# Kernel optimization log

Measured on AMD Instinct MI355X. Metric: run time of the kernel, lower is better.

The kernel has to match this reference:

```python
import jax, jax.numpy as jnp
import numpy as np

D_MODEL = 2048
N_HEADS = 32
N_KV_HEADS = 8
D_K = D_MODEL // N_HEADS          # 64
N_REP = N_HEADS // N_KV_HEADS     # 4
KV_DIM = N_KV_HEADS * D_K         # 512
B, T = 4, 2048


def setup_inputs() -> dict:
    key = jax.random.key(0)
    ks = jax.random.split(key, 9)
    s_in = 1.0 / np.sqrt(D_MODEL)
    x = jax.random.normal(ks[0], (B, T, D_MODEL), dtype=jnp.float32)
    Wq = jax.random.uniform(ks[1], (D_MODEL, D_MODEL), jnp.float32, -s_in, s_in)
    bq = jax.random.uniform(ks[2], (D_MODEL,), jnp.float32, -s_in, s_in)
    Wk = jax.random.uniform(ks[3], (D_MODEL, KV_DIM), jnp.float32, -s_in, s_in)
    bk = jax.random.uniform(ks[4], (KV_DIM,), jnp.float32, -s_in, s_in)
    Wv = jax.random.uniform(ks[5], (D_MODEL, KV_DIM), jnp.float32, -s_in, s_in)
    bv = jax.random.uniform(ks[6], (KV_DIM,), jnp.float32, -s_in, s_in)
    Wo = jax.random.uniform(ks[7], (D_MODEL, D_MODEL), jnp.float32, -s_in, s_in)
    bo = jax.random.uniform(ks[8], (D_MODEL,), jnp.float32, -s_in, s_in)
    return {"x": x, "Wq": Wq, "bq": bq, "Wk": Wk, "bk": bk,
            "Wv": Wv, "bv": bv, "Wo": Wo, "bo": bo}


def reference(x, Wq, bq, Wk, bk, Wv, bv, Wo, bo):
    Bsz, S, _ = x.shape
    # projections
    q = x @ Wq + bq                                   # (B, T, d_model)
    k = x @ Wk + bk                                   # (B, T, kv_dim)
    v = x @ Wv + bv
    # (B, n_kv, n_rep, T, d_k) for q; (B, n_kv, T, d_k) for k, v.
    # Grouping q by kv head avoids materializing repeated K/V.
    q = q.reshape(Bsz, S, N_KV_HEADS, N_REP, D_K).transpose(0, 2, 3, 1, 4)
    k = k.reshape(Bsz, S, N_KV_HEADS, D_K).transpose(0, 2, 1, 3)
    v = v.reshape(Bsz, S, N_KV_HEADS, D_K).transpose(0, 2, 1, 3)
    scale = 1.0 / np.sqrt(D_K).astype(np.float32)
    scores = jnp.einsum('bgrtd,bgsd->bgrts', q, k) * scale  # (B, n_kv, n_rep, T, T)
    causal = jnp.tril(jnp.ones((S, S), dtype=bool))
    scores = jnp.where(causal, scores, jnp.finfo(scores.dtype).min)
    p = jax.nn.softmax(scores, axis=-1)
    o = jnp.einsum('bgrts,bgsd->bgrtd', p, v)               # (B, n_kv, n_rep, T, d_k)
    o = o.transpose(0, 3, 1, 2, 4).reshape(Bsz, S, D_MODEL)
    return o @ Wo + bo
```

## Files before the change

### kernel.cpp

```cpp
#include <hip/hip_runtime.h>
#include <cstdint>
#include <cstddef>

typedef __attribute__((ext_vector_type(8))) short short8;
typedef __attribute__((ext_vector_type(4))) float f32x4;

#define D_MODEL 2048
#define KV_DIM  512
#define N_HEADS 32
#define N_KV    8
#define D_K     64
#define B_SZ    4
#define T_SEQ   2048
#define M_TOT   (B_SZ * T_SEQ)
#define N1      (D_MODEL + 2 * KV_DIM)
#define NEG_BIG (-1e30f)
#define Q_PRESCALE 0.18033688011112042f

__device__ __forceinline__ unsigned short f2bf(float f) {
    union { float f; unsigned int i; } c; c.f = f;
    unsigned int u = c.i;
    u += 0x7FFFu + ((u >> 16) & 1u);
    return (unsigned short)(u >> 16);
}

__device__ __forceinline__ unsigned int cvtpk_bf16(float lo, float hi) {
    unsigned int r;
    asm("v_cvt_pk_bf16_f32 %0, %1, %2" : "=v"(r) : "v"(lo), "v"(hi));
    return r;
}

__device__ __forceinline__ float e2(float x) {
    float r;
    asm("v_exp_f32 %0, %1" : "=v"(r) : "v"(x));
    return r;
}

__device__ __forceinline__ void async16(unsigned short* lds, const unsigned short* g) {
    __builtin_amdgcn_global_load_lds(
        (const __attribute__((address_space(1))) unsigned int*)g,
        (__attribute__((address_space(3))) unsigned int*)lds, 16, 0, 0);
}

__global__ __launch_bounds__(256)
void stage_x(const float* __restrict__ x, unsigned short* __restrict__ xb, int n) {
    for (int i = blockIdx.x * blockDim.x + threadIdx.x; i * 4 < n;
         i += gridDim.x * blockDim.x) {
        const f32x4 v = *(const f32x4*)&x[i * 4];
        unsigned short o[4];
#pragma unroll
        for (int k = 0; k < 4; k++) o[k] = f2bf(v[k]);
        *(uint64_t*)&xb[i * 4] = *(const uint64_t*)o;
    }
}

__global__ __launch_bounds__(256)
void transpose_f32_bf16(const float* __restrict__ src,
                        unsigned short* __restrict__ dst, int R, int C) {
    __shared__ unsigned short tile[32][34];
    int bx = blockIdx.x * 32;
    int by = blockIdx.y * 32;
    int tx = threadIdx.x;
    int ty = threadIdx.y;
#pragma unroll
    for (int i = 0; i < 32; i += 8)
        tile[ty + i][tx] = f2bf(src[(size_t)(by + ty + i) * C + bx + tx]);
    __syncthreads();
#pragma unroll
    for (int i = 0; i < 32; i += 8)
        dst[(size_t)(bx + ty + i) * R + by + tx] = tile[tx][ty + i];
}

template <int MODE>
__global__ __launch_bounds__(256)
void gemm_bt(const unsigned short* __restrict__ A,
             const unsigned short* __restrict__ Bt,
             const float* __restrict__ b0,
             const float* __restrict__ b1,
             const float* __restrict__ b2,
             unsigned short* __restrict__ out0,
             unsigned short* __restrict__ out1,
             unsigned short* __restrict__ out2,
             float* __restrict__ outF,
             int K) {
    __shared__ __align__(16) unsigned short As[128 * 32];
    __shared__ __align__(16) unsigned short Bs[128 * 32];

    const int t    = threadIdx.x;
    const int wave = t >> 6;
    const int lane = t & 63;
    const int quad = lane >> 4;
    const int l16  = lane & 15;
    const int wm   = (wave >> 1) * 64;
    const int wn   = (wave & 1) * 64;
    const int rowBase = blockIdx.y * 128;
    const int colBase = blockIdx.x * 128;

    f32x4 acc[4][4];
#pragma unroll
    for (int i = 0; i < 4; i++)
#pragma unroll
        for (int j = 0; j < 4; j++)
            acc[i][j] = (f32x4){0.f, 0.f, 0.f, 0.f};

    const int r0  = t >> 2;
    const int off = (t & 3) * 8;
    const unsigned short* Ap = A  + (size_t)(rowBase + r0) * K + off;
    const unsigned short* Bp = Bt + (size_t)(colBase + r0) * K + off;
    const size_t rowStep = (size_t)64 * K;

    for (int k0 = 0; k0 < K; k0 += 32) {
        *(short8*)&As[t * 8]         = *(const short8*)(Ap + k0);
        *(short8*)&As[(t + 256) * 8] = *(const short8*)(Ap + rowStep + k0);
        *(short8*)&Bs[t * 8]         = *(const short8*)(Bp + k0);
        *(short8*)&Bs[(t + 256) * 8] = *(const short8*)(Bp + rowStep + k0);
        __syncthreads();

        short8 af[4], bfr[4];
#pragma unroll
        for (int i = 0; i < 4; i++)
            af[i] = *(const short8*)&As[(wm + i * 16 + l16) * 32 + quad * 8];
#pragma unroll
        for (int i = 0; i < 4; i++)
            bfr[i] = *(const short8*)&Bs[(wn + i * 16 + l16) * 32 + quad * 8];

#pragma unroll
        for (int mi = 0; mi < 4; mi++)
#pragma unroll
            for (int ni = 0; ni < 4; ni++)
                acc[mi][ni] = __builtin_amdgcn_mfma_f32_16x16x32_bf16(
                    af[mi], bfr[ni], acc[mi][ni], 0, 0, 0);
        __syncthreads();
    }

#pragma unroll
    for (int mi = 0; mi < 4; mi++) {
        const int rowT = rowBase + wm + mi * 16 + quad * 4;
#pragma unroll
        for (int ni = 0; ni < 4; ni++) {
            const int col = colBase + wn + ni * 16 + l16;
#pragma unroll
            for (int r = 0; r < 4; r++) {
                float v = acc[mi][ni][r];
                const int rr = rowT + r;
                if (MODE == 0) {
                    if (col < D_MODEL) {
                        v = (v + b0[col]) * Q_PRESCALE;
                        out0[(size_t)rr * D_MODEL + col] = f2bf(v);
                    } else if (col < D_MODEL + KV_DIM) {
                        const int c = col - D_MODEL;
                        v += b1[c];
                        out1[(size_t)rr * KV_DIM + c] = f2bf(v);
                    } else {
                        const int c = col - (D_MODEL + KV_DIM);
                        v += b2[c];
                        const int b   = rr >> 11;
                        const int tt  = rr & 2047;
                        const int kvh = c >> 6;
                        const int d   = c & 63;
                        out2[((size_t)((b * N_KV + kvh) * D_K + d)) * T_SEQ + tt] = f2bf(v);
                    }
                } else {
                    v += b0[col];
                    outF[(size_t)rr * D_MODEL + col] = v;
                }
            }
        }
    }
}

__global__ __launch_bounds__(512)
void attn_fwd(const unsigned short* __restrict__ qb,
              const unsigned short* __restrict__ kb,
              const unsigned short* __restrict__ vt,
              unsigned short* __restrict__ ob) {
    __shared__ __align__(16) unsigned short Ks[4][64 * 64];
    __shared__ __align__(16) unsigned short Vs[4][64 * 64];

    const int t    = threadIdx.x;
    const int wave = t >> 6;
    const int lane = t & 63;
    const int quad = lane >> 4;
    const int l16  = lane & 15;
    const int qt   = (int)gridDim.x - 1 - (int)blockIdx.x;
    const int h    = blockIdx.y;
    const int b    = blockIdx.z;
    const int kvh  = h >> 2;
    const int qBase = qt * 256;
    const int rowG  = b * T_SEQ;
    const size_t vtBase = (size_t)(b * N_KV + kvh) * D_K * T_SEQ;

    short8 qf[2][2];
#pragma unroll
    for (int mi = 0; mi < 2; mi++) {
        const int row = rowG + qBase + wave * 32 + mi * 16 + l16;
#pragma unroll
        for (int kk = 0; kk < 2; kk++)
            qf[mi][kk] = *(const short8*)&qb[(size_t)row * D_MODEL + h * D_K + kk * 32 + quad * 8];
    }

    f32x4 oacc[2][4];
#pragma unroll
    for (int i = 0; i < 2; i++)
#pragma unroll
        for (int j = 0; j < 4; j++)
            oacc[i][j] = (f32x4){0.f, 0.f, 0.f, 0.f};
    float m_run[2], l_run[2];
#pragma unroll
    for (int i = 0; i < 2; i++) { m_run[i] = NEG_BIG; l_run[i] = 0.f; }

    const int rr  = t >> 3;
    const int sc8 = ((t & 7) ^ (rr & 7)) << 3;

    auto stage = [&](int bi, int sB) {
        async16(&Ks[bi][wave * 8 * 64],
                kb + (size_t)(rowG + sB + rr) * KV_DIM + kvh * D_K + sc8);
        async16(&Vs[bi][wave * 8 * 64],
                vt + vtBase + (size_t)rr * T_SEQ + sB + sc8);
    };

    const int jMax = 4 * qt + 3;

    stage(0, 0);
    stage(1, 64);
    stage(2, 128);

    for (int j = 0; j <= jMax; ++j) {
        const int rem = jMax - j;
        if (rem >= 2)      asm volatile("s_waitcnt vmcnt(4)" ::: "memory");
        else if (rem == 1) asm volatile("s_waitcnt vmcnt(2)" ::: "memory");
        else               asm volatile("s_waitcnt vmcnt(0)" ::: "memory");
        __builtin_amdgcn_s_barrier();
        __builtin_amdgcn_sched_barrier(0);

        if (rem >= 3) stage((j + 3) & 3, (j + 3) * 64);

        const int sRel = j * 64 - qBase;
        const bool skip   = sRel > wave * 32 + 31;
        const bool doMask = sRel + 63 > wave * 32;

        if (!skip) {
            const int bi = j & 3;
            const char* KsB = (const char*)&Ks[bi][0];
            const char* VsB = (const char*)&Vs[bi][0];
            const int swz   = (l16 & 7) << 4;

            f32x4 sacc[4][2];
            __builtin_amdgcn_s_setprio(1);
#pragma unroll
            for (int ni = 0; ni < 4; ni++) {
                const int rowB = (ni * 16 + l16) * 128;
                const short8 kf0 = *(const short8*)(KsB + rowB + ((quad * 16) ^ swz));
                const short8 kf1 = *(const short8*)(KsB + rowB + ((64 + quad * 16) ^ swz));
#pragma unroll
                for (int mi = 0; mi < 2; mi++) {
                    f32x4 s = (f32x4){0.f, 0.f, 0.f, 0.f};
                    s = __builtin_amdgcn_mfma_f32_16x16x32_bf16(kf0, qf[mi][0], s, 0, 0, 0);
                    s = __builtin_amdgcn_mfma_f32_16x16x32_bf16(kf1, qf[mi][1], s, 0, 0, 0);
                    sacc[ni][mi] = s;
                }
            }
            __builtin_amdgcn_s_setprio(0);

            uint2 packed[4][2];
#pragma unroll
            for (int mi = 0; mi < 2; mi++) {
                float tm = NEG_BIG;
#pragma unroll
                for (int ni = 0; ni < 4; ni++)
#pragma unroll
                    for (int r = 0; r < 4; r++) {
                        float v = sacc[ni][mi][r];
                        if (doMask) {
                            const int kc = sRel + ni * 16 + quad * 4 + r;
                            const int qr = wave * 32 + mi * 16 + l16;
                            if (kc > qr) v = NEG_BIG;
                        }
                        sacc[ni][mi][r] = v;
                        tm = fmaxf(tm, v);
                    }
                tm = fmaxf(tm, __shfl_xor(tm, 16));
                tm = fmaxf(tm, __shfl_xor(tm, 32));

                float mref = m_run[mi];
                float mnew, alpha;
                if (__all(tm <= mref + 11.0f)) {
                    mnew = mref; alpha = 1.f;
                } else {
                    mnew  = fmaxf(mref, tm);
                    alpha = e2(mref - mnew);
                    m_run[mi] = mnew;
#pragma unroll
                    for (int r2 = 0; r2 < 4; r2++) {
                        const float aR = __shfl(alpha, (lane & 48) + quad * 4 + r2);
#pragma unroll
                        for (int di = 0; di < 4; di++) oacc[mi][di][r2] *= aR;
                    }
                }
                float rs = 0.f;
#pragma unroll
                for (int ni = 0; ni < 4; ni++) {
#pragma unroll
                    for (int r = 0; r < 4; r++) {
                        const float p = e2(sacc[ni][mi][r] - mnew);
                        sacc[ni][mi][r] = p;
                        rs += p;
                    }
                    packed[ni][mi].x = cvtpk_bf16(sacc[ni][mi][0], sacc[ni][mi][1]);
                    packed[ni][mi].y = cvtpk_bf16(sacc[ni][mi][2], sacc[ni][mi][3]);
                }
                rs += __shfl_xor(rs, 16);
                rs += __shfl_xor(rs, 32);
                l_run[mi] = l_run[mi] * alpha + rs;
            }

#pragma unroll
            for (int ks = 0; ks < 2; ks++) {
                short8 pa[2];
#pragma unroll
                for (int mi = 0; mi < 2; mi++) {
                    const int srcA = ((quad & 1) << 5) + l16;
                    const uint2 pL = packed[2 * ks][mi];
                    const uint2 pH = packed[2 * ks + 1][mi];
                    const unsigned a0x = __shfl((int)pL.x, srcA);
                    const unsigned a0y = __shfl((int)pL.y, srcA);
                    const unsigned b0x = __shfl((int)pL.x, srcA + 16);
                    const unsigned b0y = __shfl((int)pL.y, srcA + 16);
                    const unsigned a1x = __shfl((int)pH.x, srcA);
                    const unsigned a1y = __shfl((int)pH.y, srcA);
                    const unsigned b1x = __shfl((int)pH.x, srcA + 16);
                    const unsigned b1y = __shfl((int)pH.y, srcA + 16);
                    const int hi = quad >> 1;
                    union { unsigned u[4]; short8 s; } pw;
                    pw.u[0] = hi ? a1x : a0x;
                    pw.u[1] = hi ? a1y : a0y;
                    pw.u[2] = hi ? b1x : b0x;
                    pw.u[3] = hi ? b1y : b0y;
                    pa[mi] = pw.s;
                }
                __builtin_amdgcn_s_setprio(1);
#pragma unroll
                for (int di = 0; di < 4; di++) {
                    const short8 vb = *(const short8*)(VsB + (di * 16 + l16) * 128 +
                                                      ((ks * 64 + quad * 16) ^ swz));
#pragma unroll
                    for (int mi = 0; mi < 2; mi++)
                        oacc[mi][di] = __builtin_amdgcn_mfma_f32_16x16x32_bf16(
                            pa[mi], vb, oacc[mi][di], 0, 0, 0);
                }
                __builtin_amdgcn_s_setprio(0);
            }
        }
    }

#pragma unroll
    for (int mi = 0; mi < 2; mi++) {
#pragma unroll
        for (int r = 0; r < 4; r++) {
            const float lr  = __shfl(l_run[mi], (lane & 48) + quad * 4 + r);
            const float inv = 1.f / lr;
            const int row = rowG + qBase + wave * 32 + mi * 16 + quad * 4 + r;
#pragma unroll
            for (int di = 0; di < 4; di++)
                ob[(size_t)row * D_MODEL + h * D_K + di * 16 + l16] =
                    f2bf(oacc[mi][di][r] * inv);
        }
    }
}

extern "C" void kernel_launch(void* const* d_in, const int* in_sizes, int n_in,
                              void* d_out, int out_size, void* d_ws, size_t ws_size,
                              hipStream_t stream) {
    const float* x  = (const float*)d_in[0];
    const float* Wq = (const float*)d_in[1];
    const float* bq = (const float*)d_in[2];
    const float* Wk = (const float*)d_in[3];
    const float* bk = (const float*)d_in[4];
    const float* Wv = (const float*)d_in[5];
    const float* bv = (const float*)d_in[6];
    const float* Wo = (const float*)d_in[7];
    const float* bo = (const float*)d_in[8];
    float* out = (float*)d_out;

    char* ws = (char*)d_ws;
    unsigned short* qb   = (unsigned short*)(ws);
    unsigned short* Wbuf = (unsigned short*)(ws + 33554432);
    unsigned short* xb   = (unsigned short*)(ws + 46137344);
    unsigned short* kb   = (unsigned short*)d_out;
    unsigned short* vt   = (unsigned short*)d_out + 4194304;

    stage_x<<<4096, 256, 0, stream>>>(x, xb, 16777216);

    dim3 tb(32, 8);
    transpose_f32_bf16<<<dim3(64, 64), tb, 0, stream>>>(Wq, Wbuf, 2048, 2048);
    transpose_f32_bf16<<<dim3(16, 64), tb, 0, stream>>>(Wk, Wbuf + 2048 * 2048, 2048, 512);
    transpose_f32_bf16<<<dim3(16, 64), tb, 0, stream>>>(Wv, Wbuf + 2560 * 2048, 2048, 512);

    gemm_bt<0><<<dim3(N1 / 128, M_TOT / 128), 256, 0, stream>>>(
        xb, Wbuf, bq, bk, bv, qb, kb, vt, nullptr, D_MODEL);

    transpose_f32_bf16<<<dim3(64, 64), tb, 0, stream>>>(Wo, Wbuf, 2048, 2048);

    attn_fwd<<<dim3(T_SEQ / 256, N_HEADS, B_SZ), 512, 0, stream>>>(qb, kb, vt, qb);

    gemm_bt<1><<<dim3(D_MODEL / 128, M_TOT / 128), 256, 0, stream>>>(
        qb, Wbuf, bo, nullptr, nullptr, nullptr, nullptr, nullptr, out, D_MODEL);
}
```

Before: 755.1 us.

## Remove P-operand shuffles by permuting V k-index layout, tree-reduce softmax max/sum

The probability tile was being redistributed across lanes with eight __shfl calls per MFMA operand so it matched the PV MFMA A-layout. Now each lane's own packed P values are used directly as the A operand, and the V B-operand is gathered as two 8-byte LDS reads so its k index lines up with that permuted P layout. Row max and row sum are also computed as balanced trees instead of serial chains to shorten dependency latency. This removes cross-lane permute traffic in exchange for twice as many, narrower LDS reads for V, which may raise LDS bank pressure given the swizzle.

```diff
diff --git a/kernel.cpp b/kernel.cpp
--- a/kernel.cpp
+++ b/kernel.cpp
@@ -265,20 +265,26 @@
             uint2 packed[4][2];
 #pragma unroll
             for (int mi = 0; mi < 2; mi++) {
-                float tm = NEG_BIG;
+                float v[16];
 #pragma unroll
                 for (int ni = 0; ni < 4; ni++)
 #pragma unroll
                     for (int r = 0; r < 4; r++) {
-                        float v = sacc[ni][mi][r];
+                        float x = sacc[ni][mi][r];
                         if (doMask) {
                             const int kc = sRel + ni * 16 + quad * 4 + r;
                             const int qr = wave * 32 + mi * 16 + l16;
-                            if (kc > qr) v = NEG_BIG;
+                            if (kc > qr) x = NEG_BIG;
                         }
-                        sacc[ni][mi][r] = v;
-                        tm = fmaxf(tm, v);
+                        v[ni * 4 + r] = x;
                     }
+                float m8[8];
+#pragma unroll
+                for (int i = 0; i < 8; i++) m8[i] = fmaxf(v[i], v[i + 8]);
+                float m4[4];
+#pragma unroll
+                for (int i = 0; i < 4; i++) m4[i] = fmaxf(m8[i], m8[i + 4]);
+                float tm = fmaxf(fmaxf(m4[0], m4[1]), fmaxf(m4[2], m4[3]));
                 tm = fmaxf(tm, __shfl_xor(tm, 16));
                 tm = fmaxf(tm, __shfl_xor(tm, 32));
 
@@ -297,21 +303,24 @@
                         for (int di = 0; di < 4; di++) oacc[mi][di][r2] *= aR;
                     }
                 }
-                float rs = 0.f;
-#pragma unroll
-                for (int ni = 0; ni < 4; ni++) {
-#pragma unroll
-                    for (int r = 0; r < 4; r++) {
-                        const float p = e2(sacc[ni][mi][r] - mnew);
-                        sacc[ni][mi][r] = p;
-                        rs += p;
-                    }
-                    packed[ni][mi].x = cvtpk_bf16(sacc[ni][mi][0], sacc[ni][mi][1]);
-                    packed[ni][mi].y = cvtpk_bf16(sacc[ni][mi][2], sacc[ni][mi][3]);
-                }
+                float p[16];
+#pragma unroll
+                for (int i = 0; i < 16; i++) p[i] = e2(v[i] - mnew);
+                float s8[8];
+#pragma unroll
+                for (int i = 0; i < 8; i++) s8[i] = p[i] + p[i + 8];
+                float s4[4];
+#pragma unroll
+                for (int i = 0; i < 4; i++) s4[i] = s8[i] + s8[i + 4];
+                float rs = (s4[0] + s4[1]) + (s4[2] + s4[3]);
                 rs += __shfl_xor(rs, 16);
                 rs += __shfl_xor(rs, 32);
                 l_run[mi] = l_run[mi] * alpha + rs;
+#pragma unroll
+                for (int ni = 0; ni < 4; ni++) {
+                    packed[ni][mi].x = cvtpk_bf16(p[ni * 4 + 0], p[ni * 4 + 1]);
+                    packed[ni][mi].y = cvtpk_bf16(p[ni * 4 + 2], p[ni * 4 + 3]);
+                }
             }
 
 #pragma unroll
@@ -319,34 +328,25 @@
                 short8 pa[2];
 #pragma unroll
                 for (int mi = 0; mi < 2; mi++) {
-                    const int srcA = ((quad & 1) << 5) + l16;
-                    const uint2 pL = packed[2 * ks][mi];
-                    const uint2 pH = packed[2 * ks + 1][mi];
-                    const unsigned a0x = __shfl((int)pL.x, srcA);
-                    const unsigned a0y = __shfl((int)pL.y, srcA);
-                    const unsigned b0x = __shfl((int)pL.x, srcA + 16);
-                    const unsigned b0y = __shfl((int)pL.y, srcA + 16);
-                    const unsigned a1x = __shfl((int)pH.x, srcA);
-                    const unsigned a1y = __shfl((int)pH.y, srcA);
-                    const unsigned b1x = __shfl((int)pH.x, srcA + 16);
-                    const unsigned b1y = __shfl((int)pH.y, srcA + 16);
-                    const int hi = quad >> 1;
                     union { unsigned u[4]; short8 s; } pw;
-                    pw.u[0] = hi ? a1x : a0x;
-                    pw.u[1] = hi ? a1y : a0y;
-                    pw.u[2] = hi ? b1x : b0x;
-                    pw.u[3] = hi ? b1y : b0y;
+                    pw.u[0] = packed[2 * ks][mi].x;
+                    pw.u[1] = packed[2 * ks][mi].y;
+                    pw.u[2] = packed[2 * ks + 1][mi].x;
+                    pw.u[3] = packed[2 * ks + 1][mi].y;
                     pa[mi] = pw.s;
                 }
                 __builtin_amdgcn_s_setprio(1);
 #pragma unroll
                 for (int di = 0; di < 4; di++) {
-                    const short8 vb = *(const short8*)(VsB + (di * 16 + l16) * 128 +
-                                                      ((ks * 64 + quad * 16) ^ swz));
+                    const int rowB = (di * 16 + l16) * 128;
+                    const uint2 lo = *(const uint2*)(VsB + rowB + ((ks * 64 + quad * 8) ^ swz));
+                    const uint2 hi = *(const uint2*)(VsB + rowB + ((ks * 64 + 32 + quad * 8) ^ swz));
+                    union { unsigned u[4]; short8 s; } vv;
+                    vv.u[0] = lo.x; vv.u[1] = lo.y; vv.u[2] = hi.x; vv.u[3] = hi.y;
 #pragma unroll
                     for (int mi = 0; mi < 2; mi++)
                         oacc[mi][di] = __builtin_amdgcn_mfma_f32_16x16x32_bf16(
-                            pa[mi], vb, oacc[mi][di], 0, 0, 0);
+                            pa[mi], vv.s, oacc[mi][di], 0, 0, 0);
                 }
                 __builtin_amdgcn_s_setprio(0);
             }
```

Result: faster. 720.0 us (-4.7%).
